# Performance work log

Measured on AMD Instinct MI355X. Metric: run time of the kernel, lower is better.

## Reference

```python
import jax, jax.numpy as jnp
import numpy as np

N = 50000      # nodes
E = 800000     # edges
IN_DIM = 256
HID = 96
OUT = 64
K = 2
ALPHA = 0.15
SCALING = 1.8  # NormalizedGCNConv scaling_factor
EPS = 1e-12    # torch F.normalize eps


def setup_inputs() -> dict:
    key = jax.random.key(0)
    ks = jax.random.split(key, 8)
    x = jax.random.normal(ks[0], (N, IN_DIM), jnp.float32)
    edge_index = jax.random.randint(ks[1], (2, E), 0, N, dtype=jnp.int64)
    def lin(k, fi, fo):
        s = 1.0 / np.sqrt(fi)
        kw, kb = jax.random.split(k)
        W = jax.random.uniform(kw, (fi, fo), jnp.float32, -s, s)
        b = jax.random.uniform(kb, (fo,), jnp.float32, -s, s)
        return W, b
    W0, b0 = lin(ks[2], IN_DIM, HID)   # convs[0]
    W1, b1 = lin(ks[3], HID, HID)      # convs[1]
    Wx, bx = lin(ks[4], HID, OUT)      # convx
    return {"x": x, "edge_index": edge_index,
            "W0": W0, "b0": b0, "W1": W1, "b1": b1, "Wx": Wx, "bx": bx}


def _l2norm(x):
    n = jnp.linalg.norm(x, axis=1, keepdims=True)
    return x / jnp.maximum(n, EPS)


def _gcn_norm(edge_index):
    # add self loops, symmetric normalization D^-1/2 (A+I) D^-1/2
    loop = jnp.arange(N, dtype=edge_index.dtype)
    row = jnp.concatenate([edge_index[0], loop])
    col = jnp.concatenate([edge_index[1], loop])
    deg = jax.ops.segment_sum(jnp.ones(row.shape[0], jnp.float32), col, num_segments=N)
    dinv = jnp.where(deg > 0, jax.lax.rsqrt(jnp.maximum(deg, 1.0)), 0.0)
    norm = dinv[row] * dinv[col]   # [E+N]
    return row, col, norm


def _norm_gcn_conv(x, W, b, row, col, norm):
    # linear -> L2 normalize * 1.8 -> APPNP(K, alpha), eval mode (no dropout)
    x = x @ W + b
    x = _l2norm(x) * SCALING
    h = x
    for _ in range(K):
        agg = jax.ops.segment_sum(x[row] * norm[:, None], col, num_segments=N)
        x = (1.0 - ALPHA) * agg + ALPHA * h
    return x


def reference(x, edge_index, W0, b0, W1, b1, Wx, bx):
    row, col, norm = _gcn_norm(edge_index)
    out = jax.nn.relu(_norm_gcn_conv(x, W0, b0, row, col, norm))
    # depth=3, link_len=2: loop runs i=1 only, residual condition never fires
    out = _l2norm(_norm_gcn_conv(out, W1, b1, row, col, norm)) * 1.5
    return _norm_gcn_conv(out, Wx, bx, row, col, norm)
```

## Files before the change

kernel.cpp:

```cpp
#include <hip/hip_runtime.h>
#include <hip/hip_fp16.h>
#include <math.h>

#define BETA_C 0.85f
#define ALF_C  0.15f
#define SLOTS 48

typedef _Float16 f16x8 __attribute__((ext_vector_type(8)));
typedef float f32x4 __attribute__((ext_vector_type(4)));

__global__ __launch_bounds__(256) void k_fill_tlp(
        const int* __restrict__ row, const int* __restrict__ col,
        int* __restrict__ cur, int* __restrict__ adj, int E, unsigned mulc) {
    int cls = blockIdx.x & 7;
    int e = (blockIdx.x >> 3) * 256 + threadIdx.x;
    if (e >= E) return;
    int c = col[e];
    if ((int)(((unsigned long long)(unsigned)c * mulc) >> 32) != cls) return;
    int p = atomicAdd(&cur[c], 1);
    if (p < SLOTS) adj[(size_t)c * SLOTS + p] = row[e];
}

__global__ void k_dinv_pad(const int* __restrict__ cur, float2* __restrict__ dinv2,
                           int* __restrict__ adj, int n) {
    int i = blockIdx.x * blockDim.x + threadIdx.x;
    if (i >= n) return;
    int deg = cur[i];
    float degf = (float)deg + 1.0f;
    dinv2[i] = make_float2(rsqrtf(degf), ALF_C * sqrtf(degf));
    int ds = min(deg, SLOTS);
    int d8 = (ds + 7) & ~7;
    int* ap = adj + (size_t)i * SLOTS;
    for (int p = ds; p < d8; ++p) ap[p] = i;
}

__global__ void k_prepw_all(const float* __restrict__ W0, const float* __restrict__ W1,
                            const float* __restrict__ Wx, ushort* __restrict__ WT0,
                            ushort* __restrict__ WT1, ushort* __restrict__ WTx) {
    int idx = blockIdx.x * blockDim.x + threadIdx.x;
    const int S0 = 96 * 256, S1 = 96 * 96, S2 = 64 * 96;
    const float* W; ushort* WT; int FI, FO, li;
    if (idx < S0)            { W = W0; WT = WT0; FI = 256; FO = 96; li = idx; }
    else if (idx < S0 + S1)  { W = W1; WT = WT1; FI = 96;  FO = 96; li = idx - S0; }
    else if (idx < S0+S1+S2) { W = Wx; WT = WTx; FI = 96;  FO = 64; li = idx - S0 - S1; }
    else return;
    int nrow = li / FI, k = li % FI;
    _Float16 hv = (_Float16)W[(size_t)k * FO + nrow];
    WT[li] = *(ushort*)&hv;
}

template<int FI, int FO, int ASRC_F16>
__global__ __launch_bounds__(256) void k_gemm_mfma(
        const void* __restrict__ Xv, const ushort* __restrict__ WT,
        const float* __restrict__ Bias, const float2* __restrict__ dinv2,
        ushort* __restrict__ H, int n, float scale) {
    constexpr int NT = FO / 16;
    constexpr int CPR = FI / 8;
    __shared__ ushort sA[64 * FI];
    __shared__ ushort sW[FO * FI];
    const int tid = threadIdx.x;
    const int rb = blockIdx.x * 64;

    {
        constexpr int TOT = FO * CPR;
#pragma unroll
        for (int idx = tid; idx < TOT; idx += 256) {
            int nrow = idx / CPR, c = idx % CPR;
            uint4 v = *(((const uint4*)WT) + (size_t)nrow * CPR + c);
            int byte = ((nrow * FI + c * 8) * 2) ^ ((nrow & 7) << 4);
            *(uint4*)((char*)sW + byte) = v;
        }
    }
    {
        constexpr int TOT = 64 * CPR;
#pragma unroll
        for (int idx = tid; idx < TOT; idx += 256) {
            int r = idx / CPR, c = idx % CPR;
            int gr = rb + r;
            uint4 v = make_uint4(0u, 0u, 0u, 0u);
            if (ASRC_F16) {
                if (gr < n) v = *(((const uint4*)Xv) + (size_t)gr * CPR + c);
            } else {
                if (gr < n) {
                    const float4* Xp = (const float4*)Xv;
                    float4 f0 = Xp[(size_t)gr * (FI / 4) + c * 2];
                    float4 f1 = Xp[(size_t)gr * (FI / 4) + c * 2 + 1];
                    _Float16 hv[8] = {(_Float16)f0.x, (_Float16)f0.y, (_Float16)f0.z,
                                      (_Float16)f0.w, (_Float16)f1.x, (_Float16)f1.y,
                                      (_Float16)f1.z, (_Float16)f1.w};
                    v = *(uint4*)hv;
                }
            }
            int byte = ((r * FI + c * 8) * 2) ^ ((r & 7) << 4);
            *(uint4*)((char*)sA + byte) = v;
        }
    }
    __syncthreads();

    const int lane = tid & 63;
    const int wave = tid >> 6;
    const int lcol = lane & 15;
    const int lk = lane >> 4;

    f32x4 acc[NT];
#pragma unroll
    for (int t = 0; t < NT; ++t) acc[t] = (f32x4){0.f, 0.f, 0.f, 0.f};

    const int arow = wave * 16 + lcol;
    char* sAb = (char*)sA;
    char* sWb = (char*)sW;
#pragma unroll
    for (int s = 0; s < FI / 32; ++s) {
        int abyte = ((arow * FI + s * 32 + lk * 8) * 2) ^ ((arow & 7) << 4);
        f16x8 af = *(f16x8*)(sAb + abyte);
#pragma unroll
        for (int t = 0; t < NT; ++t) {
            int nrow = t * 16 + lcol;
            int bbyte = ((nrow * FI + s * 32 + lk * 8) * 2) ^ ((nrow & 7) << 4);
            f16x8 bf = *(f16x8*)(sWb + bbyte);
            acc[t] = __builtin_amdgcn_mfma_f32_16x16x32_f16(af, bf, acc[t], 0, 0, 0);
        }
    }

    float bv[NT];
#pragma unroll
    for (int t = 0; t < NT; ++t) bv[t] = Bias[t * 16 + lcol];
    float ss[4] = {0.f, 0.f, 0.f, 0.f};
#pragma unroll
    for (int t = 0; t < NT; ++t)
#pragma unroll
        for (int r = 0; r < 4; ++r) {
            acc[t][r] += bv[t];
            ss[r] += acc[t][r] * acc[t][r];
        }
    for (int m = 1; m < 16; m <<= 1) {
#pragma unroll
        for (int r = 0; r < 4; ++r) ss[r] += __shfl_xor(ss[r], m, 64);
    }
#pragma unroll
    for (int r = 0; r < 4; ++r) {
        int grow = rb + wave * 16 + lk * 4 + r;
        if (grow < n) {
            float sc = scale * dinv2[grow].x / fmaxf(sqrtf(ss[r]), 1e-12f);
#pragma unroll
            for (int t = 0; t < NT; ++t) {
                _Float16 hv = (_Float16)(acc[t][r] * sc);
                H[(size_t)grow * FO + t * 16 + lcol] = *(ushort*)&hv;
            }
        }
    }
}

__device__ inline void unpack8(uint4 v, float* f) {
    union { uint4 u; _Float16 h[8]; } U; U.u = v;
#pragma unroll
    for (int i = 0; i < 8; ++i) f[i] = (float)U.h[i];
}

template<int C8>
__device__ inline void gather8(const uint4* __restrict__ tab,
                               const int* __restrict__ ap,
                               int d8, int j, float acc[8]) {
    for (int e = 0; e < d8; e += 8) {
        uint4 v[8];
#pragma unroll
        for (int u = 0; u < 8; ++u) v[u] = tab[(size_t)ap[e + u] * C8 + j];
#pragma unroll
        for (int u = 0; u < 8; ++u) {
            float f[8]; unpack8(v[u], f);
#pragma unroll
            for (int i = 0; i < 8; ++i) acc[i] += f[i];
        }
    }
}

template<int C8, int TPB>
__global__ __launch_bounds__(TPB) void k_prop1(
        const uint4* __restrict__ y0, uint4* __restrict__ y1,
        const int* __restrict__ adj, const int* __restrict__ cnt,
        const float2* __restrict__ dinv2, int n) {
    int tid = threadIdx.x;
    int j = tid % C8, cl = tid / C8;
    int c = blockIdx.x * (TPB / C8) + cl;
    if (c >= n) return;
    float d = dinv2[c].x;
    float a = BETA_C * d * d;
    int deg = min(cnt[c], SLOTS);
    int d8 = (deg + 7) & ~7;
    float coef_s = (a + ALF_C) - a * (float)(d8 - deg);
    const int* ap = adj + (size_t)c * SLOTS;
    float acc[8] = {0, 0, 0, 0, 0, 0, 0, 0};
    gather8<C8>(y0, ap, d8, j, acc);
    float sf[8];
    unpack8(y0[(size_t)c * C8 + j], sf);
    _Float16 hv[8];
#pragma unroll
    for (int i = 0; i < 8; ++i) hv[i] = (_Float16)(a * acc[i] + coef_s * sf[i]);
    y1[(size_t)c * C8 + j] = *(uint4*)hv;
}

template<int C8, int TPB, int ACT, int OUTF32>
__global__ __launch_bounds__(TPB) void k_prop2(
        const uint4* __restrict__ y1, const uint4* __restrict__ y0,
        void* __restrict__ out, const int* __restrict__ adj,
        const int* __restrict__ cnt, const float2* __restrict__ dinv2, int n) {
    int tid = threadIdx.x;
    int j = tid % C8, cl = tid / C8;
    int c = blockIdx.x * (TPB / C8) + cl;
    if (c >= n) return;
    float2 dv = dinv2[c];
    float a = BETA_C * dv.x;
    float t = dv.y;
    int deg = min(cnt[c], SLOTS);
    int d8 = (deg + 7) & ~7;
    float coef_s = a * (1.0f - (float)(d8 - deg));
    const int* ap = adj + (size_t)c * SLOTS;
    float acc[8] = {0, 0, 0, 0, 0, 0, 0, 0};
    gather8<C8>(y1, ap, d8, j, acc);
    float sf[8], tf[8];
    unpack8(y1[(size_t)c * C8 + j], sf);
    unpack8(y0[(size_t)c * C8 + j], tf);
    float res[8];
#pragma unroll
    for (int i = 0; i < 8; ++i) {
        res[i] = a * acc[i] + coef_s * sf[i] + t * tf[i];
        if (ACT) res[i] = fmaxf(res[i], 0.f);
    }
    if (OUTF32) {
        float4* op = (float4*)out;
        op[(size_t)c * (C8 * 2) + j * 2]     = make_float4(res[0], res[1], res[2], res[3]);
        op[(size_t)c * (C8 * 2) + j * 2 + 1] = make_float4(res[4], res[5], res[6], res[7]);
    } else {
        _Float16 hv[8];
#pragma unroll
        for (int i = 0; i < 8; ++i) hv[i] = (_Float16)res[i];
        ((uint4*)out)[(size_t)c * C8 + j] = *(uint4*)hv;
    }
}

__global__ void k_l2norm_h96(uint* __restrict__ x, int n, float scale) {
    int lane = threadIdx.x & 63, wave = threadIdx.x >> 6;
    int r = blockIdx.x * 4 + wave;
    if (r >= n) return;
    uint* p = x + (size_t)r * 48;
    float2 vf = make_float2(0.f, 0.f);
    if (lane < 48) {
        uint v = p[lane];
        union { uint u; _Float16 h[2]; } U; U.u = v;
        vf.x = (float)U.h[0]; vf.y = (float)U.h[1];
    }
    float ss = vf.x * vf.x + vf.y * vf.y;
    for (int m = 1; m < 64; m <<= 1) ss += __shfl_xor(ss, m, 64);
    float sc = scale / fmaxf(sqrtf(ss), 1e-12f);
    if (lane < 48) {
        union { uint u; _Float16 h[2]; } U;
        U.h[0] = (_Float16)(vf.x * sc); U.h[1] = (_Float16)(vf.y * sc);
        p[lane] = U.u;
    }
}

extern "C" void kernel_launch(void* const* d_in, const int* in_sizes, int n_in,
                              void* d_out, int out_size, void* d_ws, size_t ws_size,
                              hipStream_t stream) {
    const float* x  = (const float*)d_in[0];
    const int*   ei = (const int*)d_in[1];
    const float* W0 = (const float*)d_in[2];
    const float* b0 = (const float*)d_in[3];
    const float* W1 = (const float*)d_in[4];
    const float* b1 = (const float*)d_in[5];
    const float* Wx = (const float*)d_in[6];
    const float* bx = (const float*)d_in[7];
    float* out = (float*)d_out;

    const int N = in_sizes[0] / 256;
    const int E = in_sizes[1] / 2;
    const int* row = ei;
    const int* col = ei + E;

    char* ws = (char*)d_ws;
    size_t off = 0;
    auto alloc = [&](size_t bytes) -> char* {
        char* p = ws + off;
        off += (bytes + 255) & ~(size_t)255;
        return p;
    };
    int*    cur   = (int*)alloc((size_t)N * 4);
    float2* dinv2 = (float2*)alloc((size_t)N * 8);
    int*    adj   = (int*)alloc((size_t)N * SLOTS * 4);
    ushort* WT0   = (ushort*)alloc((size_t)96 * 256 * 2);
    ushort* WT1   = (ushort*)alloc((size_t)96 * 96 * 2);
    ushort* WTx   = (ushort*)alloc((size_t)64 * 96 * 2);
    ushort* Hh    = (ushort*)alloc((size_t)N * 96 * 2);
    ushort* T1h   = (ushort*)alloc((size_t)N * 96 * 2);
    ushort* T2h   = (ushort*)alloc((size_t)N * 96 * 2);
    (void)ws_size; (void)n_in; (void)out_size;

    unsigned mulc = (unsigned)((((unsigned long long)8 << 32) + (unsigned)N - 1) / (unsigned)N);

    hipMemsetAsync(cur, 0, (size_t)N * 4, stream);
    {
        int chunks = (E + 255) / 256;
        k_fill_tlp<<<chunks * 8, 256, 0, stream>>>(row, col, cur, adj, E, mulc);
    }
    k_dinv_pad<<<(N + 255) / 256, 256, 0, stream>>>(cur, dinv2, adj, N);
    {
        int tot = 96 * 256 + 96 * 96 + 64 * 96;
        k_prepw_all<<<(tot + 255) / 256, 256, 0, stream>>>(W0, W1, Wx, WT0, WT1, WTx);
    }

    int gblk = (N + 63) / 64;
    int gp12 = (N + 15) / 16;
    int gp8  = (N + 31) / 32;

    k_gemm_mfma<256, 96, 0><<<gblk, 256, 0, stream>>>(x, WT0, b0, dinv2, Hh, N, 1.8f);
    k_prop1<12, 192><<<gp12, 192, 0, stream>>>(
        (const uint4*)Hh, (uint4*)T1h, adj, cur, dinv2, N);
    k_prop2<12, 192, 1, 0><<<gp12, 192, 0, stream>>>(
        (const uint4*)T1h, (const uint4*)Hh, T2h, adj, cur, dinv2, N);

    k_gemm_mfma<96, 96, 1><<<gblk, 256, 0, stream>>>(T2h, WT1, b1, dinv2, Hh, N, 1.8f);
    k_prop1<12, 192><<<gp12, 192, 0, stream>>>(
        (const uint4*)Hh, (uint4*)T1h, adj, cur, dinv2, N);
    k_prop2<12, 192, 0, 0><<<gp12, 192, 0, stream>>>(
        (const uint4*)T1h, (const uint4*)Hh, T2h, adj, cur, dinv2, N);
    k_l2norm_h96<<<(N + 3) / 4, 256, 0, stream>>>((uint*)T2h, N, 1.5f);

    k_gemm_mfma<96, 64, 1><<<gblk, 256, 0, stream>>>(T2h, WTx, bx, dinv2, Hh, N, 1.8f);
    k_prop1<8, 256><<<gp8, 256, 0, stream>>>(
        (const uint4*)Hh, (uint4*)T1h, adj, cur, dinv2, N);
    k_prop2<8, 256, 0, 1><<<gp8, 256, 0, stream>>>(
        (const uint4*)T1h, (const uint4*)Hh, out, adj, cur, dinv2, N);
}
```

Measured before the change: 231.2 us.

## Fuse prep kernels and l2norm into prop2, gather in fp16 with padding to four

Merges the degree/pad and weight-transpose kernels into one launch, and folds the standalone L2-normalize pass into the second propagation kernel via a shared-memory row reduction. Neighbor padding drops from multiples of 8 to multiples of 4, which cuts wasted self-gathers, and adjacency indices are loaded as int4. Accumulation in the gather moves from fp32 to packed fp16 vector adds split across two accumulators. This lowers ALU work and launch count, but fp16 accumulation over up to 48 neighbors reduces accuracy.

```diff
diff --git a/kernel.cpp b/kernel.cpp
--- a/kernel.cpp
+++ b/kernel.cpp
@@ -8,6 +8,8 @@
 
 typedef _Float16 f16x8 __attribute__((ext_vector_type(8)));
 typedef float f32x4 __attribute__((ext_vector_type(4)));
+
+__device__ inline f16x8 as_h8(uint4 v) { union { uint4 u; f16x8 h; } U; U.u = v; return U.h; }
 
 __global__ __launch_bounds__(256) void k_fill_tlp(
         const int* __restrict__ row, const int* __restrict__ col,
@@ -21,32 +23,32 @@
     if (p < SLOTS) adj[(size_t)c * SLOTS + p] = row[e];
 }
 
-__global__ void k_dinv_pad(const int* __restrict__ cur, float2* __restrict__ dinv2,
-                           int* __restrict__ adj, int n) {
-    int i = blockIdx.x * blockDim.x + threadIdx.x;
-    if (i >= n) return;
-    int deg = cur[i];
-    float degf = (float)deg + 1.0f;
-    dinv2[i] = make_float2(rsqrtf(degf), ALF_C * sqrtf(degf));
-    int ds = min(deg, SLOTS);
-    int d8 = (ds + 7) & ~7;
-    int* ap = adj + (size_t)i * SLOTS;
-    for (int p = ds; p < d8; ++p) ap[p] = i;
-}
-
-__global__ void k_prepw_all(const float* __restrict__ W0, const float* __restrict__ W1,
-                            const float* __restrict__ Wx, ushort* __restrict__ WT0,
-                            ushort* __restrict__ WT1, ushort* __restrict__ WTx) {
+__global__ void k_prep(const int* __restrict__ cur, float2* __restrict__ dinv2,
+                       int* __restrict__ adj, int n, int t0,
+                       const float* __restrict__ W0, const float* __restrict__ W1,
+                       const float* __restrict__ Wx, ushort* __restrict__ WT0,
+                       ushort* __restrict__ WT1, ushort* __restrict__ WTx) {
     int idx = blockIdx.x * blockDim.x + threadIdx.x;
-    const int S0 = 96 * 256, S1 = 96 * 96, S2 = 64 * 96;
-    const float* W; ushort* WT; int FI, FO, li;
-    if (idx < S0)            { W = W0; WT = WT0; FI = 256; FO = 96; li = idx; }
-    else if (idx < S0 + S1)  { W = W1; WT = WT1; FI = 96;  FO = 96; li = idx - S0; }
-    else if (idx < S0+S1+S2) { W = Wx; WT = WTx; FI = 96;  FO = 64; li = idx - S0 - S1; }
-    else return;
-    int nrow = li / FI, k = li % FI;
-    _Float16 hv = (_Float16)W[(size_t)k * FO + nrow];
-    WT[li] = *(ushort*)&hv;
+    if (idx < n) {
+        int deg = cur[idx];
+        float degf = (float)deg + 1.0f;
+        dinv2[idx] = make_float2(rsqrtf(degf), ALF_C * sqrtf(degf));
+        int ds = min(deg, SLOTS);
+        int d4 = (ds + 3) & ~3;
+        int* ap = adj + (size_t)idx * SLOTS;
+        for (int p = ds; p < d4; ++p) ap[p] = idx;
+    } else if (idx >= t0) {
+        const int S0 = 96 * 256, S1 = 96 * 96, S2 = 64 * 96;
+        int li = idx - t0;
+        const float* W; ushort* WT; int FI, FO;
+        if (li < S0)           { W = W0; WT = WT0; FI = 256; FO = 96; }
+        else if (li < S0 + S1) { W = W1; WT = WT1; FI = 96;  FO = 96; li -= S0; }
+        else if (li < S0+S1+S2){ W = Wx; WT = WTx; FI = 96;  FO = 64; li -= S0 + S1; }
+        else return;
+        int nrow = li / FI, k = li % FI;
+        _Float16 hv = (_Float16)W[(size_t)k * FO + nrow];
+        WT[li] = *(ushort*)&hv;
+    }
 }
 
 template<int FI, int FO, int ASRC_F16>
@@ -158,19 +160,33 @@
 }
 
 template<int C8>
-__device__ inline void gather8(const uint4* __restrict__ tab,
-                               const int* __restrict__ ap,
-                               int d8, int j, float acc[8]) {
-    for (int e = 0; e < d8; e += 8) {
-        uint4 v[8];
-#pragma unroll
-        for (int u = 0; u < 8; ++u) v[u] = tab[(size_t)ap[e + u] * C8 + j];
-#pragma unroll
-        for (int u = 0; u < 8; ++u) {
-            float f[8]; unpack8(v[u], f);
-#pragma unroll
-            for (int i = 0; i < 8; ++i) acc[i] += f[i];
-        }
+__device__ inline void gather_h(const uint4* __restrict__ tab,
+                                const int* __restrict__ ap,
+                                int d4, int j, f16x8& A0, f16x8& A1) {
+    const int4* ap4 = (const int4*)ap;
+    int e = 0;
+    for (; e + 8 <= d4; e += 8) {
+        int4 a0 = ap4[e >> 2];
+        int4 a1 = ap4[(e >> 2) + 1];
+        uint4 v0 = tab[(size_t)(unsigned)a0.x * C8 + j];
+        uint4 v1 = tab[(size_t)(unsigned)a0.y * C8 + j];
+        uint4 v2 = tab[(size_t)(unsigned)a0.z * C8 + j];
+        uint4 v3 = tab[(size_t)(unsigned)a0.w * C8 + j];
+        uint4 v4 = tab[(size_t)(unsigned)a1.x * C8 + j];
+        uint4 v5 = tab[(size_t)(unsigned)a1.y * C8 + j];
+        uint4 v6 = tab[(size_t)(unsigned)a1.z * C8 + j];
+        uint4 v7 = tab[(size_t)(unsigned)a1.w * C8 + j];
+        A0 += (as_h8(v0) + as_h8(v1)) + (as_h8(v2) + as_h8(v3));
+        A1 += (as_h8(v4) + as_h8(v5)) + (as_h8(v6) + as_h8(v7));
+    }
+    if (e < d4) {
+        int4 a0 = ap4[e >> 2];
+        uint4 v0 = tab[(size_t)(unsigned)a0.x * C8 + j];
+        uint4 v1 = tab[(size_t)(unsigned)a0.y * C8 + j];
+        uint4 v2 = tab[(size_t)(unsigned)a0.z * C8 + j];
+        uint4 v3 = tab[(size_t)(unsigned)a0.w * C8 + j];
+        A0 += as_h8(v0) + as_h8(v1);
+        A1 += as_h8(v2) + as_h8(v3);
     }
 }
 
@@ -183,50 +199,77 @@
     int j = tid % C8, cl = tid / C8;
     int c = blockIdx.x * (TPB / C8) + cl;
     if (c >= n) return;
+    uint4 sv = y0[(size_t)c * C8 + j];
     float d = dinv2[c].x;
     float a = BETA_C * d * d;
     int deg = min(cnt[c], SLOTS);
-    int d8 = (deg + 7) & ~7;
-    float coef_s = (a + ALF_C) - a * (float)(d8 - deg);
-    const int* ap = adj + (size_t)c * SLOTS;
-    float acc[8] = {0, 0, 0, 0, 0, 0, 0, 0};
-    gather8<C8>(y0, ap, d8, j, acc);
+    int d4 = (deg + 3) & ~3;
+    float coef_s = (a + ALF_C) - a * (float)(d4 - deg);
+    f16x8 A0 = {0, 0, 0, 0, 0, 0, 0, 0};
+    f16x8 A1 = {0, 0, 0, 0, 0, 0, 0, 0};
+    gather_h<C8>(y0, adj + (size_t)c * SLOTS, d4, j, A0, A1);
     float sf[8];
-    unpack8(y0[(size_t)c * C8 + j], sf);
+    unpack8(sv, sf);
     _Float16 hv[8];
 #pragma unroll
-    for (int i = 0; i < 8; ++i) hv[i] = (_Float16)(a * acc[i] + coef_s * sf[i]);
+    for (int i = 0; i < 8; ++i) {
+        float acc = (float)A0[i] + (float)A1[i];
+        hv[i] = (_Float16)(a * acc + coef_s * sf[i]);
+    }
     y1[(size_t)c * C8 + j] = *(uint4*)hv;
 }
 
-template<int C8, int TPB, int ACT, int OUTF32>
+template<int C8, int TPB, int ACT, int OUTF32, int NORM>
 __global__ __launch_bounds__(TPB) void k_prop2(
         const uint4* __restrict__ y1, const uint4* __restrict__ y0,
         void* __restrict__ out, const int* __restrict__ adj,
-        const int* __restrict__ cnt, const float2* __restrict__ dinv2, int n) {
+        const int* __restrict__ cnt, const float2* __restrict__ dinv2,
+        int n, float nscale) {
+    __shared__ float ssh[NORM ? TPB : 1];
     int tid = threadIdx.x;
     int j = tid % C8, cl = tid / C8;
     int c = blockIdx.x * (TPB / C8) + cl;
-    if (c >= n) return;
-    float2 dv = dinv2[c];
-    float a = BETA_C * dv.x;
-    float t = dv.y;
-    int deg = min(cnt[c], SLOTS);
-    int d8 = (deg + 7) & ~7;
-    float coef_s = a * (1.0f - (float)(d8 - deg));
-    const int* ap = adj + (size_t)c * SLOTS;
-    float acc[8] = {0, 0, 0, 0, 0, 0, 0, 0};
-    gather8<C8>(y1, ap, d8, j, acc);
-    float sf[8], tf[8];
-    unpack8(y1[(size_t)c * C8 + j], sf);
-    unpack8(y0[(size_t)c * C8 + j], tf);
-    float res[8];
-#pragma unroll
-    for (int i = 0; i < 8; ++i) {
-        res[i] = a * acc[i] + coef_s * sf[i] + t * tf[i];
-        if (ACT) res[i] = fmaxf(res[i], 0.f);
-    }
-    if (OUTF32) {
+    if (!NORM && c >= n) return;
+    bool on = !NORM || c < n;
+    float res[8] = {0, 0, 0, 0, 0, 0, 0, 0};
+    if (on) {
+        uint4 sv1 = y1[(size_t)c * C8 + j];
+        uint4 sv0 = y0[(size_t)c * C8 + j];
+        float2 dv = dinv2[c];
+        float a = BETA_C * dv.x;
+        float t = dv.y;
+        int deg = min(cnt[c], SLOTS);
+        int d4 = (deg + 3) & ~3;
+        float coef_s = a * (1.0f - (float)(d4 - deg));
+        f16x8 A0 = {0, 0, 0, 0, 0, 0, 0, 0};
+        f16x8 A1 = {0, 0, 0, 0, 0, 0, 0, 0};
+        gather_h<C8>(y1, adj + (size_t)c * SLOTS, d4, j, A0, A1);
+        float sf[8], tf[8];
+        unpack8(sv1, sf);
+        unpack8(sv0, tf);
+#pragma unroll
+        for (int i = 0; i < 8; ++i) {
+            float acc = (float)A0[i] + (float)A1[i];
+            res[i] = a * acc + coef_s * sf[i] + t * tf[i];
+            if (ACT) res[i] = fmaxf(res[i], 0.f);
+        }
+    }
+    if (NORM) {
+        float part = 0.f;
+#pragma unroll
+        for (int i = 0; i < 8; ++i) part += res[i] * res[i];
+        ssh[tid] = part;
+        __syncthreads();
+        if (!on) return;
+        float tot = 0.f;
+#pragma unroll
+        for (int q = 0; q < C8; ++q) tot += ssh[cl * C8 + q];
+        float sc = nscale / fmaxf(sqrtf(tot), 1e-12f);
+        _Float16 hv[8];
+#pragma unroll
+        for (int i = 0; i < 8; ++i) hv[i] = (_Float16)(res[i] * sc);
+        ((uint4*)out)[(size_t)c * C8 + j] = *(uint4*)hv;
+    } else if (OUTF32) {
         float4* op = (float4*)out;
         op[(size_t)c * (C8 * 2) + j * 2]     = make_float4(res[0], res[1], res[2], res[3]);
         op[(size_t)c * (C8 * 2) + j * 2 + 1] = make_float4(res[4], res[5], res[6], res[7]);
@@ -235,27 +278,6 @@
 #pragma unroll
         for (int i = 0; i < 8; ++i) hv[i] = (_Float16)res[i];
         ((uint4*)out)[(size_t)c * C8 + j] = *(uint4*)hv;
-    }
-}
-
-__global__ void k_l2norm_h96(uint* __restrict__ x, int n, float scale) {
-    int lane = threadIdx.x & 63, wave = threadIdx.x >> 6;
-    int r = blockIdx.x * 4 + wave;
-    if (r >= n) return;
-    uint* p = x + (size_t)r * 48;
-    float2 vf = make_float2(0.f, 0.f);
-    if (lane < 48) {
-        uint v = p[lane];
-        union { uint u; _Float16 h[2]; } U; U.u = v;
-        vf.x = (float)U.h[0]; vf.y = (float)U.h[1];
-    }
-    float ss = vf.x * vf.x + vf.y * vf.y;
-    for (int m = 1; m < 64; m <<= 1) ss += __shfl_xor(ss, m, 64);
-    float sc = scale / fmaxf(sqrtf(ss), 1e-12f);
-    if (lane < 48) {
-        union { uint u; _Float16 h[2]; } U;
-        U.h[0] = (_Float16)(vf.x * sc); U.h[1] = (_Float16)(vf.y * sc);
-        p[lane] = U.u;
     }
 }
 
@@ -302,10 +324,11 @@
         int chunks = (E + 255) / 256;
         k_fill_tlp<<<chunks * 8, 256, 0, stream>>>(row, col, cur, adj, E, mulc);
     }
-    k_dinv_pad<<<(N + 255) / 256, 256, 0, stream>>>(cur, dinv2, adj, N);
     {
-        int tot = 96 * 256 + 96 * 96 + 64 * 96;
-        k_prepw_all<<<(tot + 255) / 256, 256, 0, stream>>>(W0, W1, Wx, WT0, WT1, WTx);
+        int t0 = ((N + 255) / 256) * 256;
+        int tot = t0 + 96 * 256 + 96 * 96 + 64 * 96;
+        k_prep<<<(tot + 255) / 256, 256, 0, stream>>>(cur, dinv2, adj, N, t0,
+                                                      W0, W1, Wx, WT0, WT1, WTx);
     }
 
     int gblk = (N + 63) / 64;
@@ -315,19 +338,18 @@
     k_gemm_mfma<256, 96, 0><<<gblk, 256, 0, stream>>>(x, WT0, b0, dinv2, Hh, N, 1.8f);
     k_prop1<12, 192><<<gp12, 192, 0, stream>>>(
         (const uint4*)Hh, (uint4*)T1h, adj, cur, dinv2, N);
-    k_prop2<12, 192, 1, 0><<<gp12, 192, 0, stream>>>(
-        (const uint4*)T1h, (const uint4*)Hh, T2h, adj, cur, dinv2, N);
+    k_prop2<12, 192, 1, 0, 0><<<gp12, 192, 0, stream>>>(
+        (const uint4*)T1h, (const uint4*)Hh, T2h, adj, cur, dinv2, N, 0.f);
 
     k_gemm_mfma<96, 96, 1><<<gblk, 256, 0, stream>>>(T2h, WT1, b1, dinv2, Hh, N, 1.8f);
     k_prop1<12, 192><<<gp12, 192, 0, stream>>>(
         (const uint4*)Hh, (uint4*)T1h, adj, cur, dinv2, N);
-    k_prop2<12, 192, 0, 0><<<gp12, 192, 0, stream>>>(
-        (const uint4*)T1h, (const uint4*)Hh, T2h, adj, cur, dinv2, N);
-    k_l2norm_h96<<<(N + 3) / 4, 256, 0, stream>>>((uint*)T2h, N, 1.5f);
+    k_prop2<12, 192, 0, 0, 1><<<gp12, 192, 0, stream>>>(
+        (const uint4*)T1h, (const uint4*)Hh, T2h, adj, cur, dinv2, N, 1.5f);
 
     k_gemm_mfma<96, 64, 1><<<gblk, 256, 0, stream>>>(T2h, WTx, bx, dinv2, Hh, N, 1.8f);
     k_prop1<8, 256><<<gp8, 256, 0, stream>>>(
         (const uint4*)Hh, (uint4*)T1h, adj, cur, dinv2, N);
-    k_prop2<8, 256, 0, 1><<<gp8, 256, 0, stream>>>(
-        (const uint4*)T1h, (const uint4*)Hh, out, adj, cur, dinv2, N);
-}
+    k_prop2<8, 256, 0, 1, 0><<<gp8, 256, 0, stream>>>(
+        (const uint4*)T1h, (const uint4*)Hh, out, adj, cur, dinv2, N, 0.f);
+}
```

Result: faster. 219.1 us (-5.2%).
